# Optimization experiments

Hardware: AMD Instinct MI355X
Metric: run time of the kernel (lower is better)

Reference implementation:

```python
import jax, jax.numpy as jnp
import numpy as np

B, S, D, H = 4, 2048, 1024, 16
HD = D // H

def setup_inputs() -> dict:
    key = jax.random.key(0)
    k1, k2, k3, k4, k5 = jax.random.split(key, 5)
    sc = 1.0 / np.sqrt(D)
    return {
        "x": jax.random.normal(k1, (B, S, D), dtype=jnp.float32),
        "w_qkv": jax.random.normal(k2, (D, 3 * D), dtype=jnp.float32) * sc,
        "b_qkv": jnp.zeros((3 * D,), dtype=jnp.float32),
        "w_proj": jax.random.normal(k3, (D, D), dtype=jnp.float32) * sc,
        "b_proj": jnp.zeros((D,), dtype=jnp.float32),
    }

def reference(x, w_qkv, b_qkv, w_proj, b_proj):
    bsz, seq_len, dim = x.shape
    qkv = x @ w_qkv + b_qkv                      # [B,S,3D]
    q, k, v = jnp.split(qkv, 3, axis=2)
    q = q.reshape(bsz, seq_len, H, HD).transpose(0, 2, 1, 3)  # [B,H,S,hd]
    k = k.reshape(bsz, seq_len, H, HD).transpose(0, 2, 1, 3)
    v = v.reshape(bsz, seq_len, H, HD).transpose(0, 2, 1, 3)
    att = jnp.einsum('bhqd,bhkd->bhqk', q, k) * (1.0 / np.sqrt(HD))
    causal = jnp.tril(jnp.ones((seq_len, seq_len), dtype=bool))
    att = jnp.where(causal[None, None], att, -jnp.inf)
    att = jax.nn.softmax(att, axis=-1)
    y = jnp.einsum('bhqk,bhkd->bhqd', att, v)
    y = y.transpose(0, 2, 1, 3).reshape(bsz, seq_len, dim)
    return y @ w_proj + b_proj
```

## Files before the change

### kernel.cpp

```cpp
#include <hip/hip_runtime.h>
#include <cstdint>
#include <cstddef>

typedef float  f32x4  __attribute__((ext_vector_type(4)));
typedef __bf16 bf16x8 __attribute__((ext_vector_type(8)));
typedef __bf16 bf16x4 __attribute__((ext_vector_type(4)));

#define DEVI static __device__ __forceinline__

DEVI f32x4 mfma_bf16(bf16x8 a, bf16x8 b, f32x4 c) {
  return __builtin_amdgcn_mfma_f32_16x16x32_bf16(a, b, c, 0, 0, 0);
}

DEVI void gload_lds16(const void* g, void* l) {
  __builtin_amdgcn_global_load_lds(
      (const __attribute__((address_space(1))) void*)g,
      (__attribute__((address_space(3))) void*)l, 16, 0, 0);
}

__global__ void k_cast_bf16(const float* __restrict__ src, __bf16* __restrict__ dst, int n4) {
  int i = blockIdx.x * blockDim.x + threadIdx.x;
  if (i < n4) {
    float4 v = reinterpret_cast<const float4*>(src)[i];
    bf16x4 r;
    r.x = (__bf16)v.x; r.y = (__bf16)v.y; r.z = (__bf16)v.z; r.w = (__bf16)v.w;
    reinterpret_cast<bf16x4*>(dst)[i] = r;
  }
}

__global__ void k_transpose_cast(const float* __restrict__ src, __bf16* __restrict__ dst,
                                 int R, int C) {
  __shared__ __bf16 tile[64][65];
  const int tx = threadIdx.x & 63, ty = threadIdx.x >> 6;
  const int r0 = blockIdx.y * 64, c0 = blockIdx.x * 64;
#pragma unroll
  for (int i = 0; i < 16; ++i) {
    int r = ty * 16 + i;
    tile[r][tx] = (__bf16)src[(size_t)(r0 + r) * C + c0 + tx];
  }
  __syncthreads();
#pragma unroll
  for (int i = 0; i < 16; ++i) {
    int c = ty * 16 + i;
    dst[(size_t)(c0 + c) * R + r0 + tx] = tile[tx][c];
  }
}

template <int MODE>
__global__ __launch_bounds__(256, 2) void k_gemm_bt(
    const __bf16* __restrict__ A, const __bf16* __restrict__ Bt,
    const float* __restrict__ bias, void* __restrict__ Cv,
    __bf16* __restrict__ VT,
    int M, int N, int K, int nbx) {
  __shared__ __bf16 As[128 * 64];
  __shared__ __bf16 Bs[128 * 64];
  const int t = threadIdx.x;
  const int w = t >> 6, lane = t & 63;
  const int l15 = lane & 15, lg = lane >> 4;
  const int m0 = (blockIdx.x / nbx) * 128;
  const int n0 = (blockIdx.x % nbx) * 128;
  const int wr = w >> 1, wc = w & 1;
  const int lrow = lane >> 3, lslot = lane & 7;

  f32x4 acc[4][4] = {};

  const int nK = K >> 6;
  for (int kt = 0; kt < nK; ++kt) {
    const __bf16* Ab = A + (size_t)m0 * K + kt * 64;
    const __bf16* Bb = Bt + (size_t)n0 * K + kt * 64;
#pragma unroll
    for (int c = 0; c < 4; ++c) {
      int seg = w * 4 + c;
      int row = seg * 8 + lrow;
      int cb = (lslot ^ (row & 7)) << 4;
      gload_lds16((const char*)(Ab + (size_t)row * K) + cb, (char*)As + seg * 1024);
      gload_lds16((const char*)(Bb + (size_t)row * K) + cb, (char*)Bs + seg * 1024);
    }
    __syncthreads();
#pragma unroll
    for (int ks = 0; ks < 2; ++ks) {
      bf16x8 af[4], bfr[4];
      const int cb = ks * 64 + (lg << 4);
#pragma unroll
      for (int m = 0; m < 4; ++m) {
        int row = wr * 64 + m * 16 + l15;
        af[m] = *(const bf16x8*)((const char*)As + row * 128 + (cb ^ ((row & 7) << 4)));
      }
#pragma unroll
      for (int n = 0; n < 4; ++n) {
        int row = wc * 64 + n * 16 + l15;
        bfr[n] = *(const bf16x8*)((const char*)Bs + row * 128 + (cb ^ ((row & 7) << 4)));
      }
#pragma unroll
      for (int m = 0; m < 4; ++m)
#pragma unroll
        for (int n = 0; n < 4; ++n)
          acc[m][n] = mfma_bf16(af[m], bfr[n], acc[m][n]);
    }
    __syncthreads();
  }

  const bool vsec = (MODE == 0) && (VT != nullptr) && (n0 >= 2048);
#pragma unroll
  for (int n = 0; n < 4; ++n) {
    const int gcol = n0 + wc * 64 + n * 16 + l15;
    const float bv = bias ? bias[gcol] : 0.0f;
#pragma unroll
    for (int m = 0; m < 4; ++m) {
      const int grow = m0 + wr * 64 + m * 16 + (lg << 2);
      if (vsec) {
        const int hd = gcol - 2048;
        const int b = grow >> 11, s0v = grow & 2047;
        bf16x4 pk;
#pragma unroll
        for (int r = 0; r < 4; ++r) pk[r] = (__bf16)(acc[m][n][r] + bv);
        *(bf16x4*)(VT + ((size_t)(b * 16) * 64 + hd) * 2048 + s0v) = pk;
      } else {
#pragma unroll
        for (int r = 0; r < 4; ++r) {
          float v = acc[m][n][r] + bv;
          if (MODE == 0)
            ((__bf16*)Cv)[(size_t)(grow + r) * N + gcol] = (__bf16)v;
          else
            ((float*)Cv)[(size_t)(grow + r) * N + gcol] = v;
        }
      }
    }
  }
}

__global__ __launch_bounds__(512, 2) void k_attn(
    const __bf16* __restrict__ qkv,
    const __bf16* __restrict__ VT,
    __bf16* __restrict__ Y) {
  __shared__ __bf16 kbuf[2][64 * 64];
  __shared__ __bf16 vbuf[2][64 * 64];
  __shared__ __bf16 p_lds[8][1024];
  const int t = threadIdx.x, w = t >> 6, lane = t & 63;
  const int l15 = lane & 15, lg = lane >> 4;
  const int bid = blockIdx.x;
  const int qt = 15 - (bid >> 6);
  const int bh = bid & 63;
  const int b = bh >> 4, h = bh & 15;
  const int q0 = qt * 128;
  const int nkv = 2 * qt + 2;
  const float SCL = 0.125f * 1.44269504f;

  const size_t qrow = (size_t)(b * 2048 + q0 + w * 16 + l15);
  const bf16x8 qf0 = *(const bf16x8*)(qkv + qrow * 3072 + h * 64 + lg * 8);
  const bf16x8 qf1 = *(const bf16x8*)(qkv + qrow * 3072 + h * 64 + 32 + lg * 8);

  const __bf16* kg = qkv + (size_t)(b * 2048) * 3072 + 1024 + h * 64;
  const __bf16* vg = VT + (size_t)bh * 64 * 2048;

  const int srow = t >> 3, sslot = t & 7;
  const int sb = (sslot ^ (srow & 7)) << 4;
  auto stage = [&](int bi, int kvi) {
    gload_lds16((const char*)(kg + (size_t)(kvi * 64 + srow) * 3072) + sb,
                (char*)kbuf[bi] + w * 1024);
    gload_lds16((const char*)(vg + (size_t)srow * 2048 + kvi * 64) + sb,
                (char*)vbuf[bi] + w * 1024);
  };

  f32x4 o[4] = {};
  float mr = -1e30f, lr = 0.0f;
  __bf16* pl = &p_lds[w][0];

  stage(0, 0);
  asm volatile("s_waitcnt vmcnt(0)" ::: "memory");
  __syncthreads();

  for (int kv = 0; kv < nkv; ++kv) {
    if (kv + 1 < nkv) stage((kv + 1) & 1, kv + 1);
    const char* kb = (const char*)kbuf[kv & 1];
    const char* vb = (const char*)vbuf[kv & 1];

    f32x4 s[4] = {};
    __builtin_amdgcn_s_setprio(1);
#pragma unroll
    for (int nb = 0; nb < 4; ++nb) {
      int row = nb * 16 + l15;
      int sw = (row & 7) << 4;
      bf16x8 k0 = *(const bf16x8*)(kb + row * 128 + ((lg * 16) ^ sw));
      bf16x8 k1 = *(const bf16x8*)(kb + row * 128 + ((64 + lg * 16) ^ sw));
      s[nb] = mfma_bf16(k0, qf0, s[nb]);
      s[nb] = mfma_bf16(k1, qf1, s[nb]);
    }
    __builtin_amdgcn_s_setprio(0);

    if (((kv + 1) << 6) > q0 + w * 16) {
      const int qg = q0 + w * 16 + l15;
#pragma unroll
      for (int nb = 0; nb < 4; ++nb)
#pragma unroll
        for (int r = 0; r < 4; ++r)
          if (kv * 64 + nb * 16 + lg * 4 + r > qg) s[nb][r] = -1e30f;
    }

    float pm = -3e38f;
#pragma unroll
    for (int nb = 0; nb < 4; ++nb)
      pm = fmaxf(pm, fmaxf(fmaxf(s[nb][0], s[nb][1]), fmaxf(s[nb][2], s[nb][3])));
    pm = fmaxf(pm, __shfl_xor(pm, 16));
    pm = fmaxf(pm, __shfl_xor(pm, 32));
    pm *= SCL;

    if (!__all(pm <= mr + 8.0f)) {
      float nm = fmaxf(mr, pm);
      float alpha = __builtin_amdgcn_exp2f(mr - nm);
      lr *= alpha;
      mr = nm;
#pragma unroll
      for (int r = 0; r < 4; ++r) {
        float aO = __shfl(alpha, lg * 4 + r);
        o[0][r] *= aO; o[1][r] *= aO; o[2][r] *= aO; o[3][r] *= aO;
      }
    }

    float ps = 0.0f;
    bf16x4 pk[4];
#pragma unroll
    for (int nb = 0; nb < 4; ++nb) {
      f32x4 pe;
#pragma unroll
      for (int r = 0; r < 4; ++r)
        pe[r] = __builtin_amdgcn_exp2f(fmaf(s[nb][r], SCL, -mr));
      ps += (pe[0] + pe[1]) + (pe[2] + pe[3]);
      pk[nb][0] = (__bf16)pe[0]; pk[nb][1] = (__bf16)pe[1];
      pk[nb][2] = (__bf16)pe[2]; pk[nb][3] = (__bf16)pe[3];
    }
    ps += __shfl_xor(ps, 16);
    ps += __shfl_xor(ps, 32);
    lr += ps;

    {
      const int rowb = l15 * 128;
      const int sw = (l15 & 7) << 4;
#pragma unroll
      for (int nb = 0; nb < 4; ++nb) {
        int cb = (nb * 32 + lg * 8) ^ sw;
        *(bf16x4*)((char*)pl + rowb + cb) = pk[nb];
      }
    }
    asm volatile("s_waitcnt lgkmcnt(0)" ::: "memory");
    bf16x8 pf0, pf1;
    {
      const int rowb = l15 * 128;
      const int sw = (l15 & 7) << 4;
      pf0 = *(const bf16x8*)((const char*)pl + rowb + ((lg << 4) ^ sw));
      pf1 = *(const bf16x8*)((const char*)pl + rowb + ((64 + (lg << 4)) ^ sw));
    }
    __builtin_amdgcn_s_setprio(1);
#pragma unroll
    for (int nb = 0; nb < 4; ++nb) {
      int row = nb * 16 + l15;
      int sw = (row & 7) << 4;
      bf16x8 v0 = *(const bf16x8*)(vb + row * 128 + ((lg * 16) ^ sw));
      bf16x8 v1 = *(const bf16x8*)(vb + row * 128 + ((64 + lg * 16) ^ sw));
      o[nb] = mfma_bf16(pf0, v0, o[nb]);
      o[nb] = mfma_bf16(pf1, v1, o[nb]);
    }
    __builtin_amdgcn_s_setprio(0);
    asm volatile("s_waitcnt vmcnt(0)" ::: "memory");
    __syncthreads();
  }

  float lO[4];
#pragma unroll
  for (int r = 0; r < 4; ++r) lO[r] = __shfl(lr, lg * 4 + r);
#pragma unroll
  for (int nb = 0; nb < 4; ++nb)
#pragma unroll
    for (int r = 0; r < 4; ++r) {
      float v = o[nb][r] / lO[r];
      size_t row = (size_t)(b * 2048 + q0 + w * 16 + lg * 4 + r);
      Y[row * 1024 + h * 64 + nb * 16 + l15] = (__bf16)v;
    }
}

extern "C" void kernel_launch(void* const* d_in, const int* in_sizes, int n_in,
                              void* d_out, int out_size, void* d_ws, size_t ws_size,
                              hipStream_t stream) {
  const float* x      = (const float*)d_in[0];
  const float* w_qkv  = (const float*)d_in[1];
  const float* b_qkv  = (const float*)d_in[2];
  const float* w_proj = (const float*)d_in[3];
  const float* b_proj = (const float*)d_in[4];
  float* out = (float*)d_out;

  char* ws = (char*)d_ws;
  const size_t MB = 1024 * 1024;
  __bf16* xb     = (__bf16*)(ws);
  __bf16* wqkvT  = (__bf16*)(ws + 16 * MB);
  __bf16* wprojT = (__bf16*)(ws + 22 * MB);
  __bf16* qkv    = (__bf16*)(ws + 24 * MB);
  __bf16* VT     = (__bf16*)(ws + 72 * MB);
  __bf16* Y      = (__bf16*)(ws + 88 * MB);

  k_cast_bf16<<<8192, 256, 0, stream>>>(x, xb, 8192 * 1024 / 4);
  k_transpose_cast<<<dim3(48, 16), 256, 0, stream>>>(w_qkv, wqkvT, 1024, 3072);
  k_transpose_cast<<<dim3(16, 16), 256, 0, stream>>>(w_proj, wprojT, 1024, 1024);
  k_gemm_bt<0><<<dim3(64 * 24), 256, 0, stream>>>(xb, wqkvT, b_qkv, qkv, VT, 8192, 3072, 1024, 24);
  k_attn<<<dim3(1024), 512, 0, stream>>>(qkv, VT, Y);
  k_gemm_bt<1><<<dim3(64 * 8), 256, 0, stream>>>(Y, wprojT, b_proj, out, nullptr, 8192, 1024, 1024, 8);
}
```

Measured before the change: 173.8 us.

## Permute V^T sequence layout so softmax P feeds MFMA directly from registers

The QKV GEMM epilogue now writes the transposed V with a permuted sequence order within each 64-token block. That ordering matches the register layout of the softmax probabilities, so the attention kernel can build its MFMA A-operands by concatenating register fragments. This drops the per-wave LDS round trip for P (writes, a wait and reads) and frees 16 KB of shared memory. The cost is a more complex scatter index in the GEMM epilogue, and the result is only correct if the permutation exactly matches the MFMA k-index mapping.

```diff
diff --git a/kernel.cpp b/kernel.cpp
--- a/kernel.cpp
+++ b/kernel.cpp
@@ -111,10 +111,14 @@
       if (vsec) {
         const int hd = gcol - 2048;
         const int b = grow >> 11, s0v = grow & 2047;
-        bf16x4 pk;
-#pragma unroll
-        for (int r = 0; r < 4; ++r) pk[r] = (__bf16)(acc[m][n][r] + bv);
-        *(bf16x4*)(VT + ((size_t)(b * 16) * 64 + hd) * 2048 + s0v) = pk;
+        const int nib = (s0v >> 2) & 15;
+        const int nib2 = (nib < 4) ? 2 * nib : (nib < 8) ? 2 * nib - 7
+                        : (nib < 12) ? 2 * nib - 8 : 2 * nib - 15;
+        const int sp = (s0v & ~63) | (nib2 << 2);
+        bf16x4 pkv;
+#pragma unroll
+        for (int r = 0; r < 4; ++r) pkv[r] = (__bf16)(acc[m][n][r] + bv);
+        *(bf16x4*)(VT + ((size_t)(b * 16) * 64 + hd) * 2048 + sp) = pkv;
       } else {
 #pragma unroll
         for (int r = 0; r < 4; ++r) {
@@ -135,7 +139,6 @@
     __bf16* __restrict__ Y) {
   __shared__ __bf16 kbuf[2][64 * 64];
   __shared__ __bf16 vbuf[2][64 * 64];
-  __shared__ __bf16 p_lds[8][1024];
   const int t = threadIdx.x, w = t >> 6, lane = t & 63;
   const int l15 = lane & 15, lg = lane >> 4;
   const int bid = blockIdx.x;
@@ -164,7 +167,6 @@
 
   f32x4 o[4] = {};
   float mr = -1e30f, lr = 0.0f;
-  __bf16* pl = &p_lds[w][0];
 
   stage(0, 0);
   asm volatile("s_waitcnt vmcnt(0)" ::: "memory");
@@ -233,23 +235,8 @@
     ps += __shfl_xor(ps, 32);
     lr += ps;
 
-    {
-      const int rowb = l15 * 128;
-      const int sw = (l15 & 7) << 4;
-#pragma unroll
-      for (int nb = 0; nb < 4; ++nb) {
-        int cb = (nb * 32 + lg * 8) ^ sw;
-        *(bf16x4*)((char*)pl + rowb + cb) = pk[nb];
-      }
-    }
-    asm volatile("s_waitcnt lgkmcnt(0)" ::: "memory");
-    bf16x8 pf0, pf1;
-    {
-      const int rowb = l15 * 128;
-      const int sw = (l15 & 7) << 4;
-      pf0 = *(const bf16x8*)((const char*)pl + rowb + ((lg << 4) ^ sw));
-      pf1 = *(const bf16x8*)((const char*)pl + rowb + ((64 + (lg << 4)) ^ sw));
-    }
+    const bf16x8 pf0 = __builtin_shufflevector(pk[0], pk[1], 0, 1, 2, 3, 4, 5, 6, 7);
+    const bf16x8 pf1 = __builtin_shufflevector(pk[2], pk[3], 0, 1, 2, 3, 4, 5, 6, 7);
     __builtin_amdgcn_s_setprio(1);
 #pragma unroll
     for (int nb = 0; nb < 4; ++nb) {
```

Result: no change. 171.2 us (-1.5%).
